# Performance work log

Hardware: AMD Instinct MI355X
Metric: run time of the kernel (lower is better)

## Reference

```python
import jax, jax.numpy as jnp
import numpy as np

B, N, D2, S = 64, 4096, 128, 512  # b, n, 2*d, size_s


def setup_inputs() -> dict:
    key = jax.random.key(0)
    k1, k2, k3, k4 = jax.random.split(key, 4)
    s_past = jax.random.randint(k1, (B, N), 0, S)
    yq = jax.random.normal(k2, (B, 1, D2), dtype=jnp.float32)
    y_past = jax.random.normal(k3, (B, N, D2), dtype=jnp.float32)
    w_mat = jax.random.normal(k4, (D2, D2), dtype=jnp.float32)
    return {"s_past": s_past, "yq": yq, "y_past": y_past, "w_mat": w_mat, "size_s": S}


def reference(s_past, yq, y_past, w_mat, size_s):
    # attn_logits[b,n] = yq[b,0,:] @ w_mat @ y_past[b,n,:]
    attn_logits = jnp.einsum('bqd,de,bne->bn', yq, w_mat, y_past)
    attn = jax.nn.softmax(attn_logits, axis=-1)  # (b, n)
    b, n = s_past.shape
    # post_est[b, s] = sum_n attn[b, n] * [s_past[b, n] == s]
    # fused scatter-add instead of materializing one-hot (b, n, S)
    flat_ids = (s_past + size_s * jnp.arange(b, dtype=s_past.dtype)[:, None]).reshape(-1)
    post_est = jax.ops.segment_sum(attn.reshape(-1), flat_ids,
                                   num_segments=b * size_s).reshape(b, size_s)
    return post_est
```

## Files before the change

kernel.cpp:

```cpp
#include <hip/hip_runtime.h>
#include <math.h>

#define BB 64
#define NN 4096
#define DD 128
#define SS 512
#define CHUNKS 16
#define RPC 256
#define SUBT 4

__global__ __launch_bounds__(256) void fused_kernel(
    const float* __restrict__ y_past, const float* __restrict__ yq,
    const float* __restrict__ w, const int* __restrict__ s_past,
    float* __restrict__ bins_g, float* __restrict__ pmax) {
    int b = blockIdx.x, chunk = blockIdx.y;
    int t = threadIdx.x;

    __shared__ float4 ytile[64 * 33];
    __shared__ float syq[DD];
    __shared__ float qsh[DD];
    __shared__ float bins[SS];
    __shared__ int   ssh[RPC];
    __shared__ float wred[8];

    if (t < DD) syq[t] = yq[b * DD + t];
    bins[t] = 0.f;
    bins[t + 256] = 0.f;
    ssh[t] = s_past[b * NN + chunk * RPC + t];
    __syncthreads();

    if (t < DD) {
        float acc = 0.f;
#pragma unroll
        for (int d = 0; d < DD; ++d) acc = fmaf(syq[d], w[d * DD + t], acc);
        qsh[t] = acc;
    }
    __syncthreads();

    int j = t & 3;
    int r = t >> 2;
    float4 qreg[8];
#pragma unroll
    for (int k = 0; k < 8; ++k) qreg[k] = ((const float4*)qsh)[j * 8 + k];

    const float4* gp =
        (const float4*)y_past + ((size_t)b * NN + (size_t)chunk * RPC) * 32;

    float pv[SUBT];
#pragma unroll
    for (int s = 0; s < SUBT; ++s) {
#pragma unroll
        for (int k = 0; k < 8; ++k) {
            int idx = t + k * 256;
            int rr = idx >> 5, cc = idx & 31;
            ytile[rr * 33 + cc] = gp[s * 2048 + idx];
        }
        __syncthreads();

        float4 acc = {0.f, 0.f, 0.f, 0.f};
#pragma unroll
        for (int k = 0; k < 8; ++k) {
            float4 yv = ytile[r * 33 + j * 8 + k];
            acc.x = fmaf(qreg[k].x, yv.x, acc.x);
            acc.y = fmaf(qreg[k].y, yv.y, acc.y);
            acc.z = fmaf(qreg[k].z, yv.z, acc.z);
            acc.w = fmaf(qreg[k].w, yv.w, acc.w);
        }
        float p = (acc.x + acc.y) + (acc.z + acc.w);
        p += __shfl_xor(p, 1, 64);
        p += __shfl_xor(p, 2, 64);
        pv[s] = p;
        __syncthreads();
    }

    float m = fmaxf(fmaxf(pv[0], pv[1]), fmaxf(pv[2], pv[3]));
#pragma unroll
    for (int off = 32; off > 0; off >>= 1) m = fmaxf(m, __shfl_xor(m, off, 64));
    int wave = t >> 6, lane = t & 63;
    if (lane == 0) wred[wave] = m;
    __syncthreads();
    m = fmaxf(fmaxf(wred[0], wred[1]), fmaxf(wred[2], wred[3]));

    if (j == 0) {
#pragma unroll
        for (int s = 0; s < SUBT; ++s)
            atomicAdd(&bins[ssh[s * 64 + r]], __expf(pv[s] - m));
    }
    __syncthreads();

    float* bg = bins_g + ((size_t)b * CHUNKS + chunk) * SS;
    bg[t] = bins[t];
    bg[t + 256] = bins[t + 256];
    if (t == 0) pmax[b * CHUNKS + chunk] = m;
}

__global__ __launch_bounds__(512) void combine_kernel(
    const float* __restrict__ bins_g, const float* __restrict__ pmax,
    float* __restrict__ out) {
    int b = blockIdx.x;
    int t = threadIdx.x;
    __shared__ float scale[CHUNKS];
    __shared__ float red[8];
    __shared__ float sInv;

    if (t < CHUNKS) scale[t] = pmax[b * CHUNKS + t];
    __syncthreads();
    if (t == 0) {
        float M = scale[0];
#pragma unroll
        for (int c = 1; c < CHUNKS; ++c) M = fmaxf(M, scale[c]);
#pragma unroll
        for (int c = 0; c < CHUNKS; ++c) scale[c] = __expf(scale[c] - M);
    }
    __syncthreads();

    float acc = 0.f;
#pragma unroll
    for (int c = 0; c < CHUNKS; ++c)
        acc = fmaf(bins_g[((size_t)b * CHUNKS + c) * SS + t], scale[c], acc);

    float s = acc;
#pragma unroll
    for (int off = 32; off > 0; off >>= 1) s += __shfl_xor(s, off, 64);
    if ((t & 63) == 0) red[t >> 6] = s;
    __syncthreads();
    if (t == 0) {
        float S = 0.f;
#pragma unroll
        for (int i = 0; i < 8; ++i) S += red[i];
        sInv = 1.f / S;
    }
    __syncthreads();

    out[b * SS + t] = acc * sInv;
}

extern "C" void kernel_launch(void* const* d_in, const int* in_sizes, int n_in,
                              void* d_out, int out_size, void* d_ws, size_t ws_size,
                              hipStream_t stream) {
    const int*   s_past = (const int*)d_in[0];
    const float* yq     = (const float*)d_in[1];
    const float* y_past = (const float*)d_in[2];
    const float* w_mat  = (const float*)d_in[3];

    float* ws     = (float*)d_ws;
    float* bins_g = ws;
    float* pmax   = bins_g + BB * CHUNKS * SS;
    float* out    = (float*)d_out;

    fused_kernel<<<dim3(BB, CHUNKS), 256, 0, stream>>>(y_past, yq, w_mat,
                                                       s_past, bins_g, pmax);
    combine_kernel<<<BB, SS, 0, stream>>>(bins_g, pmax, out);
}
```

Measured before the change: 205.5 us.

## Load y_past directly into registers, drop LDS tile and per-subtile barriers

Removes the shared-memory staging of y_past tiles. Each thread now reads its float4 slices straight from global memory, and the first subtile's loads are issued before the q=yq@W setup so their latency overlaps it. s_past indices are kept in registers instead of LDS, and launch bounds request 4 blocks per SM. Each thread now reads 128 contiguous bytes per row, which coalesces less well than the old staged loads. It also raises register pressure.

```diff
diff --git a/kernel.cpp b/kernel.cpp
--- a/kernel.cpp
+++ b/kernel.cpp
@@ -9,24 +9,37 @@
 #define RPC 256
 #define SUBT 4
 
-__global__ __launch_bounds__(256) void fused_kernel(
+__global__ __launch_bounds__(256, 4) void fused_kernel(
     const float* __restrict__ y_past, const float* __restrict__ yq,
     const float* __restrict__ w, const int* __restrict__ s_past,
     float* __restrict__ bins_g, float* __restrict__ pmax) {
-    int b = blockIdx.x, chunk = blockIdx.y;
-    int t = threadIdx.x;
+    const int b = blockIdx.x, chunk = blockIdx.y;
+    const int t = threadIdx.x;
+    const int j = t & 3;
+    const int r = t >> 2;
 
-    __shared__ float4 ytile[64 * 33];
     __shared__ float syq[DD];
     __shared__ float qsh[DD];
     __shared__ float bins[SS];
-    __shared__ int   ssh[RPC];
     __shared__ float wred[8];
+
+    const float4* gp =
+        (const float4*)y_past + ((size_t)b * NN + (size_t)chunk * RPC) * 32;
+
+    float4 y0[4];
+#pragma unroll
+    for (int k = 0; k < 4; ++k) y0[k] = gp[(size_t)r * 32 + j * 8 + k];
+
+    int sreg[SUBT];
+    if (j == 0) {
+#pragma unroll
+        for (int s = 0; s < SUBT; ++s)
+            sreg[s] = s_past[(size_t)b * NN + chunk * RPC + s * 64 + r];
+    }
 
     if (t < DD) syq[t] = yq[b * DD + t];
     bins[t] = 0.f;
     bins[t + 256] = 0.f;
-    ssh[t] = s_past[b * NN + chunk * RPC + t];
     __syncthreads();
 
     if (t < DD) {
@@ -37,30 +50,41 @@
     }
     __syncthreads();
 
-    int j = t & 3;
-    int r = t >> 2;
     float4 qreg[8];
 #pragma unroll
     for (int k = 0; k < 8; ++k) qreg[k] = ((const float4*)qsh)[j * 8 + k];
 
-    const float4* gp =
-        (const float4*)y_past + ((size_t)b * NN + (size_t)chunk * RPC) * 32;
+    float pv[SUBT];
 
-    float pv[SUBT];
+    {
+        float4 acc = {0.f, 0.f, 0.f, 0.f};
 #pragma unroll
-    for (int s = 0; s < SUBT; ++s) {
+        for (int k = 0; k < 4; ++k) {
+            acc.x = fmaf(qreg[k].x, y0[k].x, acc.x);
+            acc.y = fmaf(qreg[k].y, y0[k].y, acc.y);
+            acc.z = fmaf(qreg[k].z, y0[k].z, acc.z);
+            acc.w = fmaf(qreg[k].w, y0[k].w, acc.w);
+        }
 #pragma unroll
-        for (int k = 0; k < 8; ++k) {
-            int idx = t + k * 256;
-            int rr = idx >> 5, cc = idx & 31;
-            ytile[rr * 33 + cc] = gp[s * 2048 + idx];
+        for (int k = 4; k < 8; ++k) {
+            float4 yv = gp[(size_t)r * 32 + j * 8 + k];
+            acc.x = fmaf(qreg[k].x, yv.x, acc.x);
+            acc.y = fmaf(qreg[k].y, yv.y, acc.y);
+            acc.z = fmaf(qreg[k].z, yv.z, acc.z);
+            acc.w = fmaf(qreg[k].w, yv.w, acc.w);
         }
-        __syncthreads();
+        float p = (acc.x + acc.y) + (acc.z + acc.w);
+        p += __shfl_xor(p, 1, 64);
+        p += __shfl_xor(p, 2, 64);
+        pv[0] = p;
+    }
 
+#pragma unroll
+    for (int s = 1; s < SUBT; ++s) {
         float4 acc = {0.f, 0.f, 0.f, 0.f};
 #pragma unroll
         for (int k = 0; k < 8; ++k) {
-            float4 yv = ytile[r * 33 + j * 8 + k];
+            float4 yv = gp[(size_t)(s * 64 + r) * 32 + j * 8 + k];
             acc.x = fmaf(qreg[k].x, yv.x, acc.x);
             acc.y = fmaf(qreg[k].y, yv.y, acc.y);
             acc.z = fmaf(qreg[k].z, yv.z, acc.z);
@@ -70,7 +94,6 @@
         p += __shfl_xor(p, 1, 64);
         p += __shfl_xor(p, 2, 64);
         pv[s] = p;
-        __syncthreads();
     }
 
     float m = fmaxf(fmaxf(pv[0], pv[1]), fmaxf(pv[2], pv[3]));
@@ -84,7 +107,7 @@
     if (j == 0) {
 #pragma unroll
         for (int s = 0; s < SUBT; ++s)
-            atomicAdd(&bins[ssh[s * 64 + r]], __expf(pv[s] - m));
+            atomicAdd(&bins[sreg[s]], __expf(pv[s] - m));
     }
     __syncthreads();
 
```

New measurement: 206.6 us. No clear change (+0.5%).
